# Kernel tuning notes

Hardware: AMD Instinct MI355X
Metric: run time of the kernel (lower is better)

Reference implementation:

```python
import jax, jax.numpy as jnp
import numpy as np

IN_CH = 128
OUT_CH = 256
KSIZE = 3
DOWN = 2
WSCALE_GAIN = 1.0
LR_MUL = 1.0
ACT_GAIN = float(np.sqrt(2.0))  # lrelu def_gain
CONV_CLAMP = 256.0
LRELU_SLOPE = 0.2


def _setup_filter():
    # upfirdn2d.setup_filter([1,3,3,1]): normalize 1D then outer product -> 2D
    f1 = jnp.asarray([1.0, 3.0, 3.0, 1.0], dtype=jnp.float32)
    f1 = f1 / jnp.sum(f1)
    f2 = jnp.outer(f1, f1)  # [4,4]
    return f2


def setup_inputs() -> dict:
    key = jax.random.key(0)
    k1, k2 = jax.random.split(key)
    x = jax.random.normal(k1, (16, IN_CH, 256, 256), dtype=jnp.float32)
    weight = jax.random.normal(k2, (OUT_CH, IN_CH, KSIZE, KSIZE), dtype=jnp.float32)
    bias = jnp.zeros((OUT_CH,), dtype=jnp.float32)
    return {"x": x, "weight": weight, "bias": bias}


def reference(x, weight, bias):
    # runtime_gain = 1.0
    fan_in = KSIZE * KSIZE * IN_CH
    wscale = WSCALE_GAIN / np.sqrt(fan_in) * LR_MUL  # use_wscale=True
    w = weight * jnp.float32(wscale)
    b = bias * jnp.float32(LR_MUL)

    # filter_padding for k=3, fh=fw=4, down=2 -> (2,2,2,2) as (left,right,top,bottom)
    pad = (KSIZE // 2 + (4 - DOWN + 1) // 2, KSIZE // 2 + (4 - DOWN) // 2)
    # upfirdn2d(x, f, down=1, padding): pad then correlate with flipped filter
    f2 = _setup_filter()
    f2 = f2[::-1, ::-1]  # flip (symmetric here, kept for faithfulness)
    C = x.shape[1]
    fk = jnp.broadcast_to(f2[None, None], (C, 1, 4, 4))  # depthwise kernel
    x = lax.pad_fn(x, pad) if False else jnp.pad(x, ((0, 0), (0, 0), (pad[1], pad[0]) if False else (pad[0], pad[1]), (pad[0], pad[1])))
    x = jax.lax.conv_general_dilated(
        x, fk, window_strides=(1, 1), padding='VALID',
        dimension_numbers=('NCHW', 'OIHW', 'NCHW'),
        feature_group_count=C)

    # strided conv2d, padding=0, stride=down
    x = jax.lax.conv_general_dilated(
        x, w, window_strides=(DOWN, DOWN), padding='VALID',
        dimension_numbers=('NCHW', 'OIHW', 'NCHW'))

    # fused bias + lrelu + gain + clamp
    x = x + b[None, :, None, None]
    x = jnp.where(x >= 0, x, x * jnp.float32(LRELU_SLOPE)) * jnp.float32(ACT_GAIN)
    x = jnp.clip(x, -jnp.float32(CONV_CLAMP), jnp.float32(CONV_CLAMP))
    return x
```

## Files before the change

kernel.cpp:

```cpp
#include <hip/hip_runtime.h>

typedef __attribute__((ext_vector_type(8))) short bf16x8;
typedef __attribute__((ext_vector_type(4))) float f32x4;
typedef __attribute__((ext_vector_type(2))) float f32x2;

static __device__ __forceinline__ unsigned short f2bf(float f) {
    union { float f; unsigned u; } v; v.f = f;
    return (unsigned short)((v.u + 0x7FFFu + ((v.u >> 16) & 1u)) >> 16);
}

__global__ void prep_weights(const float* __restrict__ w, unsigned short* __restrict__ wp) {
    int t = blockIdx.x * 256 + threadIdx.x;
    const float wscale = 0.02946278254943948f;
    int cw = t & 31;
    int oc = (t >> 5) & 255;
    int cr = t >> 13;
    int ch = cr / 9;
    int rs = cr - ch * 9;
    int r  = rs / 3;
    int s  = rs - r * 3;
    int c  = ch * 32 + cw;
    wp[t] = f2bf(w[((oc * 128 + c) * 3 + r) * 3 + s] * wscale);
}

#define FROW(row) {                                                            \
    int xr  = xr0 + (row);                                                     \
    int xrc = xr < 0 ? 0 : (xr > 255 ? 255 : xr);                              \
    float rm = (xr == xrc) ? 0.125f : 0.0f;                                    \
    const float* p = q + (xrc << 8);                                           \
    f32x4 lo; f32x2 hi;                                                        \
    __builtin_memcpy(&lo, p, 16);                                              \
    __builtin_memcpy(&hi, p + 4, 8);                                           \
    hA[(row) & 3] = (lo.x + 3.f * (lo.y + lo.z) + lo.w) * rm;                  \
    hB[(row) & 3] = (lo.y + 3.f * (lo.z + lo.w) + hi.x) * rm;                  \
    hC[(row) & 3] = (lo.z + 3.f * (lo.w + hi.x) + hi.y) * rm;                  \
}

#define SROW(row) {                                                            \
    int xr = xr0 + (row);                                                      \
    float wv0=0.f,wv1=0.f,wv2=0.f,wv3=0.f,wv4=0.f,wv5=0.f;                     \
    if ((unsigned)xr < 256u) {                                                 \
        const float* p = q + (xr << 8);                                        \
        if ((unsigned)(wc + 0) < 256u) wv0 = p[0];                             \
        if ((unsigned)(wc + 1) < 256u) wv1 = p[1];                             \
        if ((unsigned)(wc + 2) < 256u) wv2 = p[2];                             \
        if ((unsigned)(wc + 3) < 256u) wv3 = p[3];                             \
        if ((unsigned)(wc + 4) < 256u) wv4 = p[4];                             \
        if ((unsigned)(wc + 5) < 256u) wv5 = p[5];                             \
    }                                                                          \
    hA[(row) & 3] = (wv0 + 3.f * (wv1 + wv2) + wv3) * 0.125f;                  \
    hB[(row) & 3] = (wv1 + 3.f * (wv2 + wv3) + wv4) * 0.125f;                  \
    hC[(row) & 3] = (wv2 + 3.f * (wv3 + wv4) + wv5) * 0.125f;                  \
}

#define VROW(row) {                                                            \
    float bv0 = (hA[(row - 3) & 3] + 3.f * (hA[(row - 2) & 3] + hA[(row - 1) & 3]) + hA[(row) & 3]) * 0.125f; \
    float bv1 = (hB[(row - 3) & 3] + 3.f * (hB[(row - 2) & 3] + hB[(row - 1) & 3]) + hB[(row) & 3]) * 0.125f; \
    unsigned rb = (unsigned)(row - 3) * 2640u;                                 \
    *(unsigned short*)(lds + rb + o0) = f2bf(bv0);                             \
    *(unsigned short*)(lds + rb + o1) = f2bf(bv1);                             \
    if (a == 15) {                                                             \
        float bv2 = (hC[(row - 3) & 3] + 3.f * (hC[(row - 2) & 3] + hC[(row - 1) & 3]) + hC[(row) & 3]) * 0.125f; \
        *(unsigned short*)(lds + rb + o2) = f2bf(bv2);                         \
    }                                                                          \
}

__global__ __launch_bounds__(512, 4)
void conv_blur_mfma(const float* __restrict__ x, const unsigned short* __restrict__ wp,
                    const float* __restrict__ bias, float* __restrict__ out) {
    __shared__ __align__(16) unsigned char lds[17 * 33 * 80];

    const int bx = blockIdx.x;
    const int n  = bx >> 7;
    const int tt = bx & 127;
    const int u0 = (tt >> 3) * 8;
    const int v0 = (tt & 7) * 16;

    const int tid  = threadIdx.x;
    const int lane = tid & 63;
    const int wid  = tid >> 6;
    const int wm   = wid >> 2;
    const int wn   = wid & 3;
    const int g    = lane >> 4;
    const int wq   = lane & 15;

    const int a   = tid & 15;
    const int chl = tid >> 4;
    const int c0  = 2 * a;
    const int wc  = 2 * v0 - 2 + c0;
    const bool edge = (v0 == 0 && a == 0) || (v0 == 112 && a == 15);
    const float* planeBase = x + (size_t)(n * 128 + chl) * 65536;
    const int xr0 = 2 * u0 - 2;

    const unsigned chpart = (unsigned)(((chl >> 1) & 3) * 4 + (chl & 1) * 2);
    const unsigned q4 = (unsigned)(chl >> 3);
    const unsigned o0 = (unsigned)(c0 + 0) * 80u + ((q4 ^ (((unsigned)(c0 + 0) >> 3) & 3u)) << 4) + chpart;
    const unsigned o1 = (unsigned)(c0 + 1) * 80u + ((q4 ^ (((unsigned)(c0 + 1) >> 3) & 3u)) << 4) + chpart;
    const unsigned o2 = (unsigned)(c0 + 2) * 80u + ((q4 ^ (((unsigned)(c0 + 2) >> 3) & 3u)) << 4) + chpart;

    const unsigned short* wpL = wp + (size_t)(wn * 64 + wq) * 32 + g * 8;

    f32x4 acc[4][4];
    #pragma unroll
    for (int i = 0; i < 4; ++i)
        #pragma unroll
        for (int j = 0; j < 4; ++j)
            acc[i][j] = (f32x4){0.f, 0.f, 0.f, 0.f};

    for (int ch = 0; ch < 4; ++ch) {
        const float* q = planeBase + (size_t)ch * 32 * 65536 + wc;
        float hA[4], hB[4], hC[4];
        if (!edge) { FROW(0) FROW(1) FROW(2) }
        else       { SROW(0) SROW(1) SROW(2) }
        __syncthreads();
        if (!edge) {
            #pragma unroll
            for (int row = 3; row < 20; ++row) { FROW(row) VROW(row) }
        } else {
            #pragma unroll
            for (int row = 3; row < 20; ++row) { SROW(row) VROW(row) }
        }
        __syncthreads();
        const unsigned short* wpc = wpL + (size_t)ch * 9 * 8192;
        #pragma unroll 1
        for (int r = 0; r < 3; ++r) {
            #pragma unroll 1
            for (int s = 0; s < 3; ++s) {
                bf16x8 b0 = *(const bf16x8*)(wpc + 0 * 512);
                bf16x8 b1 = *(const bf16x8*)(wpc + 1 * 512);
                bf16x8 b2 = *(const bf16x8*)(wpc + 2 * 512);
                bf16x8 b3 = *(const bf16x8*)(wpc + 3 * 512);
                wpc += 8192;
                int bj = 2 * wq + s;
                unsigned cb = (unsigned)bj * 80u
                            + ((unsigned)(g ^ ((bj >> 3) & 3)) << 4);
                #pragma unroll
                for (int mf = 0; mf < 4; ++mf) {
                    int bi = 2 * (wm * 4 + mf) + r;
                    bf16x8 afrag = *(const bf16x8*)(lds + (unsigned)bi * 2640u + cb);
                    acc[mf][0] = __builtin_amdgcn_mfma_f32_16x16x32_bf16(afrag, b0, acc[mf][0], 0, 0, 0);
                    acc[mf][1] = __builtin_amdgcn_mfma_f32_16x16x32_bf16(afrag, b1, acc[mf][1], 0, 0, 0);
                    acc[mf][2] = __builtin_amdgcn_mfma_f32_16x16x32_bf16(afrag, b2, acc[mf][2], 0, 0, 0);
                    acc[mf][3] = __builtin_amdgcn_mfma_f32_16x16x32_bf16(afrag, b3, acc[mf][3], 0, 0, 0);
                }
            }
        }
    }

    const float gain = 1.4142135623730951f;
    #pragma unroll
    for (int nf = 0; nf < 4; ++nf) {
        int ocg = wn * 64 + nf * 16 + wq;
        float bv = bias[ocg];
        #pragma unroll
        for (int mf = 0; mf < 4; ++mf) {
            int u = u0 + wm * 4 + mf;
            f32x4 o;
            #pragma unroll
            for (int i = 0; i < 4; ++i) {
                float z = acc[mf][nf][i] + bv;
                z = (z >= 0.f ? z : 0.2f * z) * gain;
                o[i] = fminf(fmaxf(z, -256.f), 256.f);
            }
            *(f32x4*)(out + (((size_t)n * 256 + ocg) * 128 + u) * 128 + v0 + 4 * g) = o;
        }
    }
}

extern "C" void kernel_launch(void* const* d_in, const int* in_sizes, int n_in,
                              void* d_out, int out_size, void* d_ws, size_t ws_size,
                              hipStream_t stream) {
    const float* x    = (const float*)d_in[0];
    const float* w    = (const float*)d_in[1];
    const float* bias = (const float*)d_in[2];
    unsigned short* wp = (unsigned short*)d_ws;
    float* out = (float*)d_out;

    prep_weights<<<1152, 256, 0, stream>>>(w, wp);
    conv_blur_mfma<<<2048, 512, 0, stream>>>(x, wp, bias, out);
}
```

Before: 483.5 us.

## Split blur into separate pre-pass writing bf16 channel-interleaved tensor, pipeline conv stage

Adds a blur_pre kernel that computes the 4x4 FIR blur once per input pixel and stores it as bf16 in a swizzled channel-interleaved global buffer in workspace. A new conv_stage2 kernel stages tiles of that buffer into LDS with register prefetch of the next channel group, and double-buffers weight fragments across unrolled MFMA steps with setprio. The fused kernel is kept as a fallback when the workspace is too small. This removes the blur arithmetic repeated by every conv block and hides load latency. The cost is an extra ~270MB round trip through HBM.

```diff
diff --git a/kernel.cpp b/kernel.cpp
--- a/kernel.cpp
+++ b/kernel.cpp
@@ -3,6 +3,7 @@
 typedef __attribute__((ext_vector_type(8))) short bf16x8;
 typedef __attribute__((ext_vector_type(4))) float f32x4;
 typedef __attribute__((ext_vector_type(2))) float f32x2;
+typedef __attribute__((ext_vector_type(4))) unsigned int u32x4;
 
 static __device__ __forceinline__ unsigned short f2bf(float f) {
     union { float f; unsigned u; } v; v.f = f;
@@ -23,6 +24,261 @@
     wp[t] = f2bf(w[((oc * 128 + c) * 3 + r) * 3 + s] * wscale);
 }
 
+
+__global__ void blur_pre(const float* __restrict__ x, unsigned char* __restrict__ bl) {
+    const int b   = blockIdx.x;
+    const int tid = threadIdx.x;
+    const int c   = tid & 31;
+    if (b < 64) {
+        const int n = b >> 2, cg = b & 3;
+        const float* xp = x + (size_t)(n * 128 + cg * 32 + c) * 65536;
+        unsigned char* ob = bl + (size_t)(n * 4 + cg) * 4260096;
+        const int eb = tid >> 5;
+        const float fw0 = 1.f, fw1 = 3.f, fw2 = 3.f, fw3 = 1.f;
+        for (int e = eb; e < 513; e += 8) {
+            int t, J;
+            if (e < 257) { t = e; J = 256; } else { t = 256; J = e - 257; }
+            float acc = 0.f;
+            #pragma unroll
+            for (int p = 0; p < 4; ++p) {
+                int xr = t - 2 + p;
+                if ((unsigned)xr < 256u) {
+                    const float* rp = xp + (xr << 8);
+                    float fp = (p == 0) ? fw0 : (p == 1) ? fw1 : (p == 2) ? fw2 : fw3;
+                    #pragma unroll
+                    for (int q = 0; q < 4; ++q) {
+                        int xc = J - 2 + q;
+                        float fq = (q == 0) ? fw0 : (q == 1) ? fw1 : (q == 2) ? fw2 : fw3;
+                        if ((unsigned)xc < 256u) acc += fp * fq * rp[xc];
+                    }
+                }
+            }
+            acc *= 0.015625f;
+            unsigned off = (unsigned)(J ^ ((J >> 1) & 1)) * 64u
+                         + ((unsigned)((c >> 3) ^ ((J >> 2) & 3)) << 4) + (unsigned)(c & 7) * 2u;
+            *(unsigned short*)(ob + (size_t)t * 16512 + off) = f2bf(acc);
+        }
+        return;
+    }
+    const int b2 = b - 64;
+    const int tband = b2 & 15, band = (b2 >> 4) & 3, cg = (b2 >> 6) & 3, n = b2 >> 8;
+    const int cb = tid >> 5;
+    const int J0 = band * 64 + cb * 8;
+    const int t0 = tband * 16;
+    const bool edge = (J0 == 0) || (J0 == 248);
+    const float* xp = x + (size_t)(n * 128 + cg * 32 + c) * 65536;
+    unsigned char* ob = bl + (size_t)(n * 4 + cg) * 4260096;
+    unsigned off[8];
+    #pragma unroll
+    for (int j = 0; j < 8; ++j) {
+        int J = J0 + j;
+        off[j] = (unsigned)(J ^ ((J >> 1) & 1)) * 64u
+               + ((unsigned)((c >> 3) ^ ((J >> 2) & 3)) << 4) + (unsigned)(c & 7) * 2u;
+    }
+    float h[8][4];
+    #pragma unroll
+    for (int i = 0; i < 19; ++i) {
+        int xr = t0 - 2 + i;
+        if (!edge) {
+            int xc = xr < 0 ? 0 : (xr > 255 ? 255 : xr);
+            float rm = (xr == xc) ? 0.125f : 0.f;
+            const float* p = xp + (xc << 8) + (J0 - 2);
+            f32x4 w0, w1, w2;
+            __builtin_memcpy(&w0, p, 16);
+            __builtin_memcpy(&w1, p + 4, 16);
+            __builtin_memcpy(&w2, p + 8, 16);
+            float wv[12] = {w0.x, w0.y, w0.z, w0.w, w1.x, w1.y, w1.z, w1.w,
+                            w2.x, w2.y, w2.z, w2.w};
+            #pragma unroll
+            for (int j = 0; j < 8; ++j)
+                h[j][i & 3] = (wv[j] + 3.f * (wv[j + 1] + wv[j + 2]) + wv[j + 3]) * rm;
+        } else {
+            float wv[12];
+            #pragma unroll
+            for (int m = 0; m < 12; ++m) {
+                int xc2 = J0 - 2 + m;
+                wv[m] = ((unsigned)xr < 256u && (unsigned)xc2 < 256u)
+                        ? xp[(xr << 8) + xc2] : 0.f;
+            }
+            #pragma unroll
+            for (int j = 0; j < 8; ++j)
+                h[j][i & 3] = (wv[j] + 3.f * (wv[j + 1] + wv[j + 2]) + wv[j + 3]) * 0.125f;
+        }
+        if (i >= 3) {
+            unsigned char* rowp = ob + (size_t)(t0 + i - 3) * 16512;
+            #pragma unroll
+            for (int j = 0; j < 8; ++j) {
+                float B = (h[j][(i - 3) & 3] + 3.f * (h[j][(i - 2) & 3] + h[j][(i - 1) & 3])
+                           + h[j][i & 3]) * 0.125f;
+                *(unsigned short*)(rowp + off[j]) = f2bf(B);
+            }
+        }
+    }
+}
+
+#define MF __builtin_amdgcn_mfma_f32_16x16x32_bf16
+#define WLOAD(S0, S1, S2, S3, KOFF) {                                          \
+    const unsigned short* _wn = wbase + (size_t)(KOFF) * 8192;                 \
+    S0 = *(const bf16x8*)(_wn);        S1 = *(const bf16x8*)(_wn + 512);       \
+    S2 = *(const bf16x8*)(_wn + 1024); S3 = *(const bf16x8*)(_wn + 1536);      \
+}
+#define CSTEP(ADRS, R, S0, S1, S2, S3) {                                       \
+    const unsigned char* _ab = lds + (ADRS) + (R) * 2112;                      \
+    bf16x8 a0 = *(const bf16x8*)(_ab);                                         \
+    bf16x8 a1 = *(const bf16x8*)(_ab + 4224);                                  \
+    bf16x8 a2 = *(const bf16x8*)(_ab + 8448);                                  \
+    bf16x8 a3 = *(const bf16x8*)(_ab + 12672);                                 \
+    __builtin_amdgcn_s_setprio(1);                                             \
+    acc[0][0]=MF(a0,S0,acc[0][0],0,0,0); acc[0][1]=MF(a0,S1,acc[0][1],0,0,0);  \
+    acc[0][2]=MF(a0,S2,acc[0][2],0,0,0); acc[0][3]=MF(a0,S3,acc[0][3],0,0,0);  \
+    acc[1][0]=MF(a1,S0,acc[1][0],0,0,0); acc[1][1]=MF(a1,S1,acc[1][1],0,0,0);  \
+    acc[1][2]=MF(a1,S2,acc[1][2],0,0,0); acc[1][3]=MF(a1,S3,acc[1][3],0,0,0);  \
+    acc[2][0]=MF(a2,S0,acc[2][0],0,0,0); acc[2][1]=MF(a2,S1,acc[2][1],0,0,0);  \
+    acc[2][2]=MF(a2,S2,acc[2][2],0,0,0); acc[2][3]=MF(a2,S3,acc[2][3],0,0,0);  \
+    acc[3][0]=MF(a3,S0,acc[3][0],0,0,0); acc[3][1]=MF(a3,S1,acc[3][1],0,0,0);  \
+    acc[3][2]=MF(a3,S2,acc[3][2],0,0,0); acc[3][3]=MF(a3,S3,acc[3][3],0,0,0);  \
+    __builtin_amdgcn_s_setprio(0);                                             \
+}
+#define CHUNK(BASE, A0,A1,A2,A3, B0,B1,B2,B3)                                  \
+    CSTEP(adr0, 0, A0,A1,A2,A3) WLOAD(A0,A1,A2,A3, (BASE)+2)                   \
+    CSTEP(adr1, 0, B0,B1,B2,B3) WLOAD(B0,B1,B2,B3, (BASE)+3)                   \
+    CSTEP(adr2, 0, A0,A1,A2,A3) WLOAD(A0,A1,A2,A3, (BASE)+4)                   \
+    CSTEP(adr0, 1, B0,B1,B2,B3) WLOAD(B0,B1,B2,B3, (BASE)+5)                   \
+    CSTEP(adr1, 1, A0,A1,A2,A3) WLOAD(A0,A1,A2,A3, (BASE)+6)                   \
+    CSTEP(adr2, 1, B0,B1,B2,B3) WLOAD(B0,B1,B2,B3, (BASE)+7)                   \
+    CSTEP(adr0, 2, A0,A1,A2,A3) WLOAD(A0,A1,A2,A3, (BASE)+8)                   \
+    CSTEP(adr1, 2, B0,B1,B2,B3) WLOAD(B0,B1,B2,B3, (BASE)+9)                   \
+    CSTEP(adr2, 2, A0,A1,A2,A3) WLOAD(A0,A1,A2,A3, (BASE)+10)
+#define CHUNK_LAST(BASE, A0,A1,A2,A3, B0,B1,B2,B3)                             \
+    CSTEP(adr0, 0, A0,A1,A2,A3) WLOAD(A0,A1,A2,A3, (BASE)+2)                   \
+    CSTEP(adr1, 0, B0,B1,B2,B3) WLOAD(B0,B1,B2,B3, (BASE)+3)                   \
+    CSTEP(adr2, 0, A0,A1,A2,A3) WLOAD(A0,A1,A2,A3, (BASE)+4)                   \
+    CSTEP(adr0, 1, B0,B1,B2,B3) WLOAD(B0,B1,B2,B3, (BASE)+5)                   \
+    CSTEP(adr1, 1, A0,A1,A2,A3) WLOAD(A0,A1,A2,A3, (BASE)+6)                   \
+    CSTEP(adr2, 1, B0,B1,B2,B3) WLOAD(B0,B1,B2,B3, (BASE)+7)                   \
+    CSTEP(adr0, 2, A0,A1,A2,A3) WLOAD(A0,A1,A2,A3, (BASE)+8)                   \
+    CSTEP(adr1, 2, B0,B1,B2,B3)                                                \
+    CSTEP(adr2, 2, A0,A1,A2,A3)
+
+__global__ __launch_bounds__(512, 3)
+void conv_stage2(const unsigned char* __restrict__ bl, const unsigned short* __restrict__ wp,
+                 const float* __restrict__ bias, float* __restrict__ out) {
+    __shared__ __align__(16) unsigned char lds[35904];
+
+    const int bx = blockIdx.x;
+    const int n  = bx >> 7;
+    const int tt = bx & 127;
+    const int u0 = (tt >> 3) * 8;
+    const int v0 = (tt & 7) * 16;
+
+    const int tid  = threadIdx.x;
+    const int lane = tid & 63;
+    const int wid  = tid >> 6;
+    const int wm   = wid >> 2;
+    const int wn   = wid & 3;
+    const int g    = lane >> 4;
+    const int wq   = lane & 15;
+
+    unsigned goff[5];
+    #pragma unroll
+    for (int k = 0; k < 5; ++k) {
+        int sl  = tid + 512 * k;
+        int row = sl / 132;
+        int cs  = sl - row * 132;
+        goff[k] = (unsigned)(2 * u0 + row) * 16512u + (unsigned)v0 * 128u + (unsigned)cs * 16u;
+    }
+    const bool v4 = (tid < 196);
+    const unsigned char* gb = bl + (size_t)n * 4 * 4260096;
+
+    unsigned adr0, adr1, adr2;
+    {
+        #pragma unroll
+        for (int s = 0; s < 3; ++s) {
+            unsigned bj = 2u * (unsigned)wq + (unsigned)s;
+            unsigned av = (bj ^ ((bj >> 1) & 1u)) * 64u
+                        + (((unsigned)g ^ ((bj >> 2) & 3u)) << 4) + (unsigned)wm * 16896u;
+            if (s == 0) adr0 = av; else if (s == 1) adr1 = av; else adr2 = av;
+        }
+    }
+
+    const unsigned short* wbase = wp + (size_t)(wn * 64 + wq) * 32 + g * 8;
+    bf16x8 WA0, WA1, WA2, WA3, WB0, WB1, WB2, WB3;
+    WLOAD(WA0, WA1, WA2, WA3, 0)
+    WLOAD(WB0, WB1, WB2, WB3, 1)
+
+    f32x4 acc[4][4];
+    #pragma unroll
+    for (int i = 0; i < 4; ++i)
+        #pragma unroll
+        for (int j = 0; j < 4; ++j)
+            acc[i][j] = (f32x4){0.f, 0.f, 0.f, 0.f};
+
+    u32x4 L0, L1, L2, L3, L4 = (u32x4){0u, 0u, 0u, 0u};
+    {
+        const unsigned char* g0 = gb;
+        L0 = *(const u32x4*)(g0 + goff[0]);
+        L1 = *(const u32x4*)(g0 + goff[1]);
+        L2 = *(const u32x4*)(g0 + goff[2]);
+        L3 = *(const u32x4*)(g0 + goff[3]);
+        if (v4) L4 = *(const u32x4*)(g0 + goff[4]);
+    }
+    const unsigned lb = (unsigned)tid * 16u;
+
+#define STAGE_WRITE() {                                                        \
+    *(u32x4*)(lds + lb)          = L0;                                         \
+    *(u32x4*)(lds + lb + 8192)   = L1;                                         \
+    *(u32x4*)(lds + lb + 16384)  = L2;                                         \
+    *(u32x4*)(lds + lb + 24576)  = L3;                                         \
+    if (v4) *(u32x4*)(lds + lb + 32768) = L4;                                  \
+}
+#define STAGE_LOAD(CGN) {                                                      \
+    const unsigned char* _gn = gb + (size_t)(CGN) * 4260096;                   \
+    L0 = *(const u32x4*)(_gn + goff[0]);                                       \
+    L1 = *(const u32x4*)(_gn + goff[1]);                                       \
+    L2 = *(const u32x4*)(_gn + goff[2]);                                       \
+    L3 = *(const u32x4*)(_gn + goff[3]);                                       \
+    if (v4) L4 = *(const u32x4*)(_gn + goff[4]);                               \
+}
+
+    STAGE_WRITE()
+    __syncthreads();
+    STAGE_LOAD(1)
+    CHUNK(0, WA0, WA1, WA2, WA3, WB0, WB1, WB2, WB3)
+    __syncthreads();
+    STAGE_WRITE()
+    __syncthreads();
+    STAGE_LOAD(2)
+    CHUNK(9, WB0, WB1, WB2, WB3, WA0, WA1, WA2, WA3)
+    __syncthreads();
+    STAGE_WRITE()
+    __syncthreads();
+    STAGE_LOAD(3)
+    CHUNK(18, WA0, WA1, WA2, WA3, WB0, WB1, WB2, WB3)
+    __syncthreads();
+    STAGE_WRITE()
+    __syncthreads();
+    CHUNK_LAST(27, WB0, WB1, WB2, WB3, WA0, WA1, WA2, WA3)
+
+    const float gain = 1.4142135623730951f;
+    #pragma unroll
+    for (int nf = 0; nf < 4; ++nf) {
+        const int ocg = wn * 64 + nf * 16 + wq;
+        const float bb = bias[ocg];
+        #pragma unroll
+        for (int mf = 0; mf < 4; ++mf) {
+            int u = u0 + wm * 4 + mf;
+            f32x4 o;
+            #pragma unroll
+            for (int i = 0; i < 4; ++i) {
+                float z = acc[mf][nf][i] + bb;
+                z = (z >= 0.f ? z : 0.2f * z) * gain;
+                o[i] = fminf(fmaxf(z, -256.f), 256.f);
+            }
+            *(f32x4*)(out + (((size_t)n * 256 + ocg) * 128 + u) * 128 + v0 + 4 * g) = o;
+        }
+    }
+}
+
 #define FROW(row) {                                                            \
     int xr  = xr0 + (row);                                                     \
     int xrc = xr < 0 ? 0 : (xr > 255 ? 255 : xr);                              \
@@ -35,7 +291,6 @@
     hB[(row) & 3] = (lo.y + 3.f * (lo.z + lo.w) + hi.x) * rm;                  \
     hC[(row) & 3] = (lo.z + 3.f * (lo.w + hi.x) + hi.y) * rm;                  \
 }
-
 #define SROW(row) {                                                            \
     int xr = xr0 + (row);                                                      \
     float wv0=0.f,wv1=0.f,wv2=0.f,wv3=0.f,wv4=0.f,wv5=0.f;                     \
@@ -52,30 +307,26 @@
     hB[(row) & 3] = (wv1 + 3.f * (wv2 + wv3) + wv4) * 0.125f;                  \
     hC[(row) & 3] = (wv2 + 3.f * (wv3 + wv4) + wv5) * 0.125f;                  \
 }
-
 #define VROW(row) {                                                            \
     float bv0 = (hA[(row - 3) & 3] + 3.f * (hA[(row - 2) & 3] + hA[(row - 1) & 3]) + hA[(row) & 3]) * 0.125f; \
     float bv1 = (hB[(row - 3) & 3] + 3.f * (hB[(row - 2) & 3] + hB[(row - 1) & 3]) + hB[(row) & 3]) * 0.125f; \
     unsigned rb = (unsigned)(row - 3) * 2640u;                                 \
-    *(unsigned short*)(lds + rb + o0) = f2bf(bv0);                             \
-    *(unsigned short*)(lds + rb + o1) = f2bf(bv1);                             \
+    *(unsigned short*)(flds + rb + o0) = f2bf(bv0);                            \
+    *(unsigned short*)(flds + rb + o1) = f2bf(bv1);                            \
     if (a == 15) {                                                             \
         float bv2 = (hC[(row - 3) & 3] + 3.f * (hC[(row - 2) & 3] + hC[(row - 1) & 3]) + hC[(row) & 3]) * 0.125f; \
-        *(unsigned short*)(lds + rb + o2) = f2bf(bv2);                         \
+        *(unsigned short*)(flds + rb + o2) = f2bf(bv2);                        \
     }                                                                          \
 }
-
 __global__ __launch_bounds__(512, 4)
 void conv_blur_mfma(const float* __restrict__ x, const unsigned short* __restrict__ wp,
                     const float* __restrict__ bias, float* __restrict__ out) {
-    __shared__ __align__(16) unsigned char lds[17 * 33 * 80];
-
+    __shared__ __align__(16) unsigned char flds[17 * 33 * 80];
     const int bx = blockIdx.x;
     const int n  = bx >> 7;
     const int tt = bx & 127;
     const int u0 = (tt >> 3) * 8;
     const int v0 = (tt & 7) * 16;
-
     const int tid  = threadIdx.x;
     const int lane = tid & 63;
     const int wid  = tid >> 6;
@@ -83,30 +334,25 @@
     const int wn   = wid & 3;
     const int g    = lane >> 4;
     const int wq   = lane & 15;
-
     const int a   = tid & 15;
     const int chl = tid >> 4;
-    const int c0  = 2 * a;
-    const int wc  = 2 * v0 - 2 + c0;
+    const int wc  = 2 * v0 - 2 + 2 * a;
     const bool edge = (v0 == 0 && a == 0) || (v0 == 112 && a == 15);
     const float* planeBase = x + (size_t)(n * 128 + chl) * 65536;
     const int xr0 = 2 * u0 - 2;
-
     const unsigned chpart = (unsigned)(((chl >> 1) & 3) * 4 + (chl & 1) * 2);
     const unsigned q4 = (unsigned)(chl >> 3);
+    const int c0 = 2 * a;
     const unsigned o0 = (unsigned)(c0 + 0) * 80u + ((q4 ^ (((unsigned)(c0 + 0) >> 3) & 3u)) << 4) + chpart;
     const unsigned o1 = (unsigned)(c0 + 1) * 80u + ((q4 ^ (((unsigned)(c0 + 1) >> 3) & 3u)) << 4) + chpart;
     const unsigned o2 = (unsigned)(c0 + 2) * 80u + ((q4 ^ (((unsigned)(c0 + 2) >> 3) & 3u)) << 4) + chpart;
-
     const unsigned short* wpL = wp + (size_t)(wn * 64 + wq) * 32 + g * 8;
-
     f32x4 acc[4][4];
     #pragma unroll
     for (int i = 0; i < 4; ++i)
         #pragma unroll
         for (int j = 0; j < 4; ++j)
             acc[i][j] = (f32x4){0.f, 0.f, 0.f, 0.f};
-
     for (int ch = 0; ch < 4; ++ch) {
         const float* q = planeBase + (size_t)ch * 32 * 65536 + wc;
         float hA[4], hB[4], hC[4];
@@ -132,21 +378,19 @@
                 bf16x8 b3 = *(const bf16x8*)(wpc + 3 * 512);
                 wpc += 8192;
                 int bj = 2 * wq + s;
-                unsigned cb = (unsigned)bj * 80u
-                            + ((unsigned)(g ^ ((bj >> 3) & 3)) << 4);
+                unsigned cb = (unsigned)bj * 80u + ((unsigned)(g ^ ((bj >> 3) & 3)) << 4);
                 #pragma unroll
                 for (int mf = 0; mf < 4; ++mf) {
                     int bi = 2 * (wm * 4 + mf) + r;
-                    bf16x8 afrag = *(const bf16x8*)(lds + (unsigned)bi * 2640u + cb);
-                    acc[mf][0] = __builtin_amdgcn_mfma_f32_16x16x32_bf16(afrag, b0, acc[mf][0], 0, 0, 0);
-                    acc[mf][1] = __builtin_amdgcn_mfma_f32_16x16x32_bf16(afrag, b1, acc[mf][1], 0, 0, 0);
-                    acc[mf][2] = __builtin_amdgcn_mfma_f32_16x16x32_bf16(afrag, b2, acc[mf][2], 0, 0, 0);
-                    acc[mf][3] = __builtin_amdgcn_mfma_f32_16x16x32_bf16(afrag, b3, acc[mf][3], 0, 0, 0);
+                    bf16x8 afrag = *(const bf16x8*)(flds + (unsigned)bi * 2640u + cb);
+                    acc[mf][0] = MF(afrag, b0, acc[mf][0], 0, 0, 0);
+                    acc[mf][1] = MF(afrag, b1, acc[mf][1], 0, 0, 0);
+                    acc[mf][2] = MF(afrag, b2, acc[mf][2], 0, 0, 0);
+                    acc[mf][3] = MF(afrag, b3, acc[mf][3], 0, 0, 0);
                 }
             }
         }
     }
-
     const float gain = 1.4142135623730951f;
     #pragma unroll
     for (int nf = 0; nf < 4; ++nf) {
@@ -176,6 +420,13 @@
     unsigned short* wp = (unsigned short*)d_ws;
     float* out = (float*)d_out;
 
+    const size_t NEED = 589824u + 272646144u;
     prep_weights<<<1152, 256, 0, stream>>>(w, wp);
-    conv_blur_mfma<<<2048, 512, 0, stream>>>(x, wp, bias, out);
-}
+    if (ws_size >= NEED) {
+        unsigned char* bl = (unsigned char*)d_ws + 589824;
+        blur_pre<<<4160, 256, 0, stream>>>(x, bl);
+        conv_stage2<<<2048, 512, 0, stream>>>(bl, wp, bias, out);
+    } else {
+        conv_blur_mfma<<<2048, 512, 0, stream>>>(x, wp, bias, out);
+    }
+}
```

Result: slower. 563.2 us (+16.5%).

## Split blur into separate pass and double-buffer conv tiles via direct global-to-LDS loads

Applied to the files above, without the earlier changes.

The fused blur+conv kernel is split in two. A blur pass writes pre-swizzled bf16 tile records to workspace, and a conv kernel streams those records into double-buffered LDS with global_load_lds while running MFMAs on the previous chunk. The conv kernel also changes warp tiling to 8x2 fragments per wave, prefetches weights in registers, and raises wave priority around the MFMA bursts. This costs an extra round trip of about 294 MB through global memory, and the new path only runs if the workspace is large enough.

```diff
diff --git a/kernel.cpp b/kernel.cpp
--- a/kernel.cpp
+++ b/kernel.cpp
@@ -3,10 +3,17 @@
 typedef __attribute__((ext_vector_type(8))) short bf16x8;
 typedef __attribute__((ext_vector_type(4))) float f32x4;
 typedef __attribute__((ext_vector_type(2))) float f32x2;
+typedef __attribute__((ext_vector_type(4))) unsigned int u32x4;
 
 static __device__ __forceinline__ unsigned short f2bf(float f) {
     union { float f; unsigned u; } v; v.f = f;
     return (unsigned short)((v.u + 0x7FFFu + ((v.u >> 16) & 1u)) >> 16);
+}
+
+static __device__ __forceinline__ void g2l16(const void* g, void* l) {
+    __builtin_amdgcn_global_load_lds(
+        (const __attribute__((address_space(1))) unsigned int*)g,
+        (__attribute__((address_space(3))) unsigned int*)l, 16, 0, 0);
 }
 
 __global__ void prep_weights(const float* __restrict__ w, unsigned short* __restrict__ wp) {
@@ -23,6 +30,244 @@
     wp[t] = f2bf(w[((oc * 128 + c) * 3 + r) * 3 + s] * wscale);
 }
 
+#define BPX(ROW) {                                                             \
+    int _xr = xr0 + (ROW);                                                     \
+    int _xc = _xr < 0 ? 0 : (_xr > 255 ? 255 : _xr);                           \
+    float _rm = (_xr == _xc) ? 0.125f : 0.0f;                                  \
+    const float* _p0 = pq0 + (_xc << 8);                                       \
+    const float* _p1 = pq1 + (_xc << 8);                                       \
+    f32x4 _l0, _l1; f32x2 _h0, _h1;                                            \
+    __builtin_memcpy(&_l0, _p0, 16); __builtin_memcpy(&_h0, _p0 + 4, 8);       \
+    __builtin_memcpy(&_l1, _p1, 16); __builtin_memcpy(&_h1, _p1 + 4, 8);       \
+    hA0[(ROW) & 3] = (_l0.x + 3.f * (_l0.y + _l0.z) + _l0.w) * _rm;            \
+    hB0[(ROW) & 3] = (_l0.y + 3.f * (_l0.z + _l0.w) + _h0.x) * _rm;            \
+    hC0[(ROW) & 3] = (_l0.z + 3.f * (_l0.w + _h0.x) + _h0.y) * _rm;            \
+    hA1[(ROW) & 3] = (_l1.x + 3.f * (_l1.y + _l1.z) + _l1.w) * _rm;            \
+    hB1[(ROW) & 3] = (_l1.y + 3.f * (_l1.z + _l1.w) + _h1.x) * _rm;            \
+    hC1[(ROW) & 3] = (_l1.z + 3.f * (_l1.w + _h1.x) + _h1.y) * _rm;            \
+}
+#define BPS(ROW) {                                                             \
+    int _xr = xr0 + (ROW);                                                     \
+    float a0=0.f,a1=0.f,a2=0.f,a3=0.f,a4=0.f,a5=0.f;                           \
+    float b0=0.f,b1=0.f,b2=0.f,b3=0.f,b4=0.f,b5=0.f;                           \
+    if ((unsigned)_xr < 256u) {                                                \
+        const float* _p0 = pq0 + (_xr << 8);                                   \
+        const float* _p1 = pq1 + (_xr << 8);                                   \
+        if ((unsigned)(wc + 0) < 256u) { a0 = _p0[0]; b0 = _p1[0]; }           \
+        if ((unsigned)(wc + 1) < 256u) { a1 = _p0[1]; b1 = _p1[1]; }           \
+        if ((unsigned)(wc + 2) < 256u) { a2 = _p0[2]; b2 = _p1[2]; }           \
+        if ((unsigned)(wc + 3) < 256u) { a3 = _p0[3]; b3 = _p1[3]; }           \
+        if ((unsigned)(wc + 4) < 256u) { a4 = _p0[4]; b4 = _p1[4]; }           \
+        if ((unsigned)(wc + 5) < 256u) { a5 = _p0[5]; b5 = _p1[5]; }           \
+    }                                                                          \
+    hA0[(ROW) & 3] = (a0 + 3.f * (a1 + a2) + a3) * 0.125f;                     \
+    hB0[(ROW) & 3] = (a1 + 3.f * (a2 + a3) + a4) * 0.125f;                     \
+    hC0[(ROW) & 3] = (a2 + 3.f * (a3 + a4) + a5) * 0.125f;                     \
+    hA1[(ROW) & 3] = (b0 + 3.f * (b1 + b2) + b3) * 0.125f;                     \
+    hB1[(ROW) & 3] = (b1 + 3.f * (b2 + b3) + b4) * 0.125f;                     \
+    hC1[(ROW) & 3] = (b2 + 3.f * (b3 + b4) + b5) * 0.125f;                     \
+}
+#define BPV(ROW) {                                                             \
+    float vA0 = (hA0[(ROW-3)&3] + 3.f*(hA0[(ROW-2)&3]+hA0[(ROW-1)&3]) + hA0[(ROW)&3]) * 0.125f; \
+    float vA1 = (hA1[(ROW-3)&3] + 3.f*(hA1[(ROW-2)&3]+hA1[(ROW-1)&3]) + hA1[(ROW)&3]) * 0.125f; \
+    float vB0 = (hB0[(ROW-3)&3] + 3.f*(hB0[(ROW-2)&3]+hB0[(ROW-1)&3]) + hB0[(ROW)&3]) * 0.125f; \
+    float vB1 = (hB1[(ROW-3)&3] + 3.f*(hB1[(ROW-2)&3]+hB1[(ROW-1)&3]) + hB1[(ROW)&3]) * 0.125f; \
+    unsigned _rb = (unsigned)(ROW - 3) * 2112u;                                \
+    *(unsigned*)(blds + _rb + o0) = (unsigned)f2bf(vA0) | ((unsigned)f2bf(vA1) << 16); \
+    *(unsigned*)(blds + _rb + o1) = (unsigned)f2bf(vB0) | ((unsigned)f2bf(vB1) << 16); \
+    if (a15) {                                                                 \
+        float vC0 = (hC0[(ROW-3)&3] + 3.f*(hC0[(ROW-2)&3]+hC0[(ROW-1)&3]) + hC0[(ROW)&3]) * 0.125f; \
+        float vC1 = (hC1[(ROW-3)&3] + 3.f*(hC1[(ROW-2)&3]+hC1[(ROW-1)&3]) + hC1[(ROW)&3]) * 0.125f; \
+        *(unsigned*)(blds + _rb + o2) = (unsigned)f2bf(vC0) | ((unsigned)f2bf(vC1) << 16); \
+    }                                                                          \
+}
+#define BPF(ROW) BPX(ROW) BPV(ROW)
+#define BPP(ROW) BPS(ROW) BPV(ROW)
+
+__global__ __launch_bounds__(256, 4)
+void blur_rec(const float* __restrict__ x, unsigned char* __restrict__ bm) {
+    __shared__ __align__(16) unsigned char blds[35904];
+    const int bx   = blockIdx.x;
+    const int cg   = bx & 3;
+    const int tile = (bx >> 2) & 127;
+    const int n    = bx >> 9;
+    const int u0   = (tile >> 3) * 8;
+    const int v0   = (tile & 7) * 16;
+    const int tid  = threadIdx.x;
+    const int a    = tid & 15;
+    const int chp  = tid >> 4;
+    const bool a15 = (a == 15);
+    const int wc   = 2 * v0 - 2 + 2 * a;
+    const bool edge = (v0 == 0 && a == 0) || (v0 == 112 && a15);
+    const float* pq0 = x + (size_t)(n * 128 + cg * 32 + 2 * chp) * 65536 + wc;
+    const float* pq1 = pq0 + 65536;
+    const int xr0 = 2 * u0 - 2;
+
+    const int J0 = 2 * a, J1 = 2 * a + 1;
+    const unsigned cb2 = (unsigned)(chp & 3) * 4u;
+    const unsigned o0 = (unsigned)((J0 ^ ((J0 >> 1) & 1)) * 64) + ((((unsigned)chp >> 2) ^ (((unsigned)J0 >> 2) & 3u)) << 4) + cb2;
+    const unsigned o1 = (unsigned)((J1 ^ ((J1 >> 1) & 1)) * 64) + ((((unsigned)chp >> 2) ^ (((unsigned)J1 >> 2) & 3u)) << 4) + cb2;
+    const unsigned o2 = 2048u + (((unsigned)chp >> 2) << 4) + cb2;
+
+    {
+        float hA0[4], hB0[4], hC0[4], hA1[4], hB1[4], hC1[4];
+        if (!edge) {
+            BPX(0) BPX(1) BPX(2)
+            BPF(3)  BPF(4)  BPF(5)  BPF(6)  BPF(7)  BPF(8)  BPF(9)  BPF(10)
+            BPF(11) BPF(12) BPF(13) BPF(14) BPF(15) BPF(16) BPF(17) BPF(18) BPF(19)
+        } else {
+            BPS(0) BPS(1) BPS(2)
+            BPP(3)  BPP(4)  BPP(5)  BPP(6)  BPP(7)  BPP(8)  BPP(9)  BPP(10)
+            BPP(11) BPP(12) BPP(13) BPP(14) BPP(15) BPP(16) BPP(17) BPP(18) BPP(19)
+        }
+    }
+    __syncthreads();
+    unsigned char* dst = bm + (size_t)bx * 35904u;
+    #pragma unroll
+    for (int k = 0; k < 8; ++k)
+        *(u32x4*)(dst + (unsigned)(tid + 256 * k) * 16u) =
+            *(const u32x4*)(blds + (unsigned)(tid + 256 * k) * 16u);
+    if (tid < 196)
+        *(u32x4*)(dst + (unsigned)(tid + 2048) * 16u) =
+            *(const u32x4*)(blds + (unsigned)(tid + 2048) * 16u);
+}
+
+#define MF __builtin_amdgcn_mfma_f32_16x16x32_bf16
+#define WLOAD2(S0, S1, KOFF) {                                                 \
+    const unsigned short* _wn = wbase + (size_t)(KOFF) * 8192;                 \
+    S0 = *(const bf16x8*)(_wn); S1 = *(const bf16x8*)(_wn + 512);              \
+}
+#define CSTEP8(BUF, ADRS, R, S0, S1) {                                         \
+    const unsigned char* _ab = lds + (BUF) + (ADRS) + (R) * 2112;              \
+    bf16x8 a0 = *(const bf16x8*)(_ab);                                         \
+    bf16x8 a1 = *(const bf16x8*)(_ab +  4224);                                 \
+    bf16x8 a2 = *(const bf16x8*)(_ab +  8448);                                 \
+    bf16x8 a3 = *(const bf16x8*)(_ab + 12672);                                 \
+    bf16x8 a4 = *(const bf16x8*)(_ab + 16896);                                 \
+    bf16x8 a5 = *(const bf16x8*)(_ab + 21120);                                 \
+    bf16x8 a6 = *(const bf16x8*)(_ab + 25344);                                 \
+    bf16x8 a7 = *(const bf16x8*)(_ab + 29568);                                 \
+    __builtin_amdgcn_s_setprio(1);                                             \
+    acc[0][0]=MF(a0,S0,acc[0][0],0,0,0); acc[0][1]=MF(a0,S1,acc[0][1],0,0,0);  \
+    acc[1][0]=MF(a1,S0,acc[1][0],0,0,0); acc[1][1]=MF(a1,S1,acc[1][1],0,0,0);  \
+    acc[2][0]=MF(a2,S0,acc[2][0],0,0,0); acc[2][1]=MF(a2,S1,acc[2][1],0,0,0);  \
+    acc[3][0]=MF(a3,S0,acc[3][0],0,0,0); acc[3][1]=MF(a3,S1,acc[3][1],0,0,0);  \
+    acc[4][0]=MF(a4,S0,acc[4][0],0,0,0); acc[4][1]=MF(a4,S1,acc[4][1],0,0,0);  \
+    acc[5][0]=MF(a5,S0,acc[5][0],0,0,0); acc[5][1]=MF(a5,S1,acc[5][1],0,0,0);  \
+    acc[6][0]=MF(a6,S0,acc[6][0],0,0,0); acc[6][1]=MF(a6,S1,acc[6][1],0,0,0);  \
+    acc[7][0]=MF(a7,S0,acc[7][0],0,0,0); acc[7][1]=MF(a7,S1,acc[7][1],0,0,0);  \
+    __builtin_amdgcn_s_setprio(0);                                             \
+}
+#define CHUNK8(BUF, BASE, A0,A1, B0,B1)                                        \
+    CSTEP8(BUF, adr0, 0, A0,A1) WLOAD2(A0,A1, (BASE)+2)                        \
+    CSTEP8(BUF, adr1, 0, B0,B1) WLOAD2(B0,B1, (BASE)+3)                        \
+    CSTEP8(BUF, adr2, 0, A0,A1) WLOAD2(A0,A1, (BASE)+4)                        \
+    CSTEP8(BUF, adr0, 1, B0,B1) WLOAD2(B0,B1, (BASE)+5)                        \
+    CSTEP8(BUF, adr1, 1, A0,A1) WLOAD2(A0,A1, (BASE)+6)                        \
+    CSTEP8(BUF, adr2, 1, B0,B1) WLOAD2(B0,B1, (BASE)+7)                        \
+    CSTEP8(BUF, adr0, 2, A0,A1) WLOAD2(A0,A1, (BASE)+8)                        \
+    CSTEP8(BUF, adr1, 2, B0,B1) WLOAD2(B0,B1, (BASE)+9)                        \
+    CSTEP8(BUF, adr2, 2, A0,A1) WLOAD2(A0,A1, (BASE)+10)
+#define CHUNK8_LAST(BUF, BASE, A0,A1, B0,B1)                                   \
+    CSTEP8(BUF, adr0, 0, A0,A1) WLOAD2(A0,A1, (BASE)+2)                        \
+    CSTEP8(BUF, adr1, 0, B0,B1) WLOAD2(B0,B1, (BASE)+3)                        \
+    CSTEP8(BUF, adr2, 0, A0,A1) WLOAD2(A0,A1, (BASE)+4)                        \
+    CSTEP8(BUF, adr0, 1, B0,B1) WLOAD2(B0,B1, (BASE)+5)                        \
+    CSTEP8(BUF, adr1, 1, A0,A1) WLOAD2(A0,A1, (BASE)+6)                        \
+    CSTEP8(BUF, adr2, 1, B0,B1) WLOAD2(B0,B1, (BASE)+7)                        \
+    CSTEP8(BUF, adr0, 2, A0,A1) WLOAD2(A0,A1, (BASE)+8)                        \
+    CSTEP8(BUF, adr1, 2, B0,B1)                                                \
+    CSTEP8(BUF, adr2, 2, A0,A1)
+
+__global__ __launch_bounds__(512, 4)
+void conv_stage2(const unsigned char* __restrict__ bm, const unsigned short* __restrict__ wp,
+                 const float* __restrict__ bias, float* __restrict__ out) {
+    __shared__ __align__(16) unsigned char lds[2 * 35904];
+
+    const int bx = blockIdx.x;
+    const int n  = bx >> 7;
+    const int tt = bx & 127;
+    const int u0 = (tt >> 3) * 8;
+    const int v0 = (tt & 7) * 16;
+
+    const int tid  = threadIdx.x;
+    const int lane = tid & 63;
+    const int wid  = tid >> 6;
+    const int g    = lane >> 4;
+    const int wq   = lane & 15;
+
+    const unsigned char* rec = bm + (size_t)((n * 128 + tt) * 4) * 35904u;
+
+#define STAGE(BUF, CG) {                                                       \
+    const unsigned char* _src = rec + (size_t)(CG) * 35904u;                   \
+    _Pragma("unroll")                                                          \
+    for (int k = 0; k < 4; ++k)                                                \
+        g2l16(_src + (unsigned)(tid + 512 * k) * 16u,                          \
+              lds + (BUF) + (unsigned)(tid + 512 * k) * 16u);                  \
+    if (tid < 196)                                                             \
+        g2l16(_src + (unsigned)(tid + 2048) * 16u,                             \
+              lds + (BUF) + (unsigned)(tid + 2048) * 16u);                     \
+}
+
+    unsigned adr0, adr1, adr2;
+    {
+        #pragma unroll
+        for (int s = 0; s < 3; ++s) {
+            unsigned bj = 2u * (unsigned)wq + (unsigned)s;
+            unsigned av = (bj ^ ((bj >> 1) & 1u)) * 64u
+                        + (((unsigned)g ^ ((bj >> 2) & 3u)) << 4);
+            if (s == 0) adr0 = av; else if (s == 1) adr1 = av; else adr2 = av;
+        }
+    }
+
+    const unsigned short* wbase = wp + (size_t)(wid * 32 + wq) * 32 + g * 8;
+    bf16x8 WA0, WA1, WB0, WB1;
+    WLOAD2(WA0, WA1, 0)
+    WLOAD2(WB0, WB1, 1)
+
+    f32x4 acc[8][2];
+    #pragma unroll
+    for (int i = 0; i < 8; ++i) {
+        acc[i][0] = (f32x4){0.f, 0.f, 0.f, 0.f};
+        acc[i][1] = (f32x4){0.f, 0.f, 0.f, 0.f};
+    }
+
+    STAGE(0, 0)
+    __syncthreads();
+
+    STAGE(35904, 1)
+    CHUNK8(0, 0, WA0, WA1, WB0, WB1)
+    __syncthreads();
+
+    STAGE(0, 2)
+    CHUNK8(35904, 9, WB0, WB1, WA0, WA1)
+    __syncthreads();
+
+    STAGE(35904, 3)
+    CHUNK8(0, 18, WA0, WA1, WB0, WB1)
+    __syncthreads();
+
+    CHUNK8_LAST(35904, 27, WB0, WB1, WA0, WA1)
+
+    const float gain = 1.4142135623730951f;
+    #pragma unroll
+    for (int nf = 0; nf < 2; ++nf) {
+        const int ocg = wid * 32 + nf * 16 + wq;
+        const float bb = bias[ocg];
+        #pragma unroll
+        for (int mf = 0; mf < 8; ++mf) {
+            f32x4 o;
+            #pragma unroll
+            for (int i = 0; i < 4; ++i) {
+                float z = acc[mf][nf][i] + bb;
+                z = (z >= 0.f ? z : 0.2f * z) * gain;
+                o[i] = fminf(fmaxf(z, -256.f), 256.f);
+            }
+            *(f32x4*)(out + (((size_t)n * 256 + ocg) * 128 + (u0 + mf)) * 128 + v0 + 4 * g) = o;
+        }
+    }
+}
+
 #define FROW(row) {                                                            \
     int xr  = xr0 + (row);                                                     \
     int xrc = xr < 0 ? 0 : (xr > 255 ? 255 : xr);                              \
@@ -35,7 +280,6 @@
     hB[(row) & 3] = (lo.y + 3.f * (lo.z + lo.w) + hi.x) * rm;                  \
     hC[(row) & 3] = (lo.z + 3.f * (lo.w + hi.x) + hi.y) * rm;                  \
 }
-
 #define SROW(row) {                                                            \
     int xr = xr0 + (row);                                                      \
     float wv0=0.f,wv1=0.f,wv2=0.f,wv3=0.f,wv4=0.f,wv5=0.f;                     \
@@ -52,30 +296,26 @@
     hB[(row) & 3] = (wv1 + 3.f * (wv2 + wv3) + wv4) * 0.125f;                  \
     hC[(row) & 3] = (wv2 + 3.f * (wv3 + wv4) + wv5) * 0.125f;                  \
 }
-
 #define VROW(row) {                                                            \
     float bv0 = (hA[(row - 3) & 3] + 3.f * (hA[(row - 2) & 3] + hA[(row - 1) & 3]) + hA[(row) & 3]) * 0.125f; \
     float bv1 = (hB[(row - 3) & 3] + 3.f * (hB[(row - 2) & 3] + hB[(row - 1) & 3]) + hB[(row) & 3]) * 0.125f; \
     unsigned rb = (unsigned)(row - 3) * 2640u;                                 \
-    *(unsigned short*)(lds + rb + o0) = f2bf(bv0);                             \
-    *(unsigned short*)(lds + rb + o1) = f2bf(bv1);                             \
+    *(unsigned short*)(flds + rb + o0) = f2bf(bv0);                            \
+    *(unsigned short*)(flds + rb + o1) = f2bf(bv1);                            \
     if (a == 15) {                                                             \
         float bv2 = (hC[(row - 3) & 3] + 3.f * (hC[(row - 2) & 3] + hC[(row - 1) & 3]) + hC[(row) & 3]) * 0.125f; \
-        *(unsigned short*)(lds + rb + o2) = f2bf(bv2);                         \
+        *(unsigned short*)(flds + rb + o2) = f2bf(bv2);                        \
     }                                                                          \
 }
-
 __global__ __launch_bounds__(512, 4)
 void conv_blur_mfma(const float* __restrict__ x, const unsigned short* __restrict__ wp,
                     const float* __restrict__ bias, float* __restrict__ out) {
-    __shared__ __align__(16) unsigned char lds[17 * 33 * 80];
-
+    __shared__ __align__(16) unsigned char flds[17 * 33 * 80];
     const int bx = blockIdx.x;
     const int n  = bx >> 7;
     const int tt = bx & 127;
     const int u0 = (tt >> 3) * 8;
     const int v0 = (tt & 7) * 16;
-
     const int tid  = threadIdx.x;
     const int lane = tid & 63;
     const int wid  = tid >> 6;
@@ -83,30 +323,25 @@
     const int wn   = wid & 3;
     const int g    = lane >> 4;
     const int wq   = lane & 15;
-
     const int a   = tid & 15;
     const int chl = tid >> 4;
-    const int c0  = 2 * a;
-    const int wc  = 2 * v0 - 2 + c0;
+    const int wc  = 2 * v0 - 2 + 2 * a;
     const bool edge = (v0 == 0 && a == 0) || (v0 == 112 && a == 15);
     const float* planeBase = x + (size_t)(n * 128 + chl) * 65536;
     const int xr0 = 2 * u0 - 2;
-
     const unsigned chpart = (unsigned)(((chl >> 1) & 3) * 4 + (chl & 1) * 2);
     const unsigned q4 = (unsigned)(chl >> 3);
+    const int c0 = 2 * a;
     const unsigned o0 = (unsigned)(c0 + 0) * 80u + ((q4 ^ (((unsigned)(c0 + 0) >> 3) & 3u)) << 4) + chpart;
     const unsigned o1 = (unsigned)(c0 + 1) * 80u + ((q4 ^ (((unsigned)(c0 + 1) >> 3) & 3u)) << 4) + chpart;
     const unsigned o2 = (unsigned)(c0 + 2) * 80u + ((q4 ^ (((unsigned)(c0 + 2) >> 3) & 3u)) << 4) + chpart;
-
     const unsigned short* wpL = wp + (size_t)(wn * 64 + wq) * 32 + g * 8;
-
     f32x4 acc[4][4];
     #pragma unroll
     for (int i = 0; i < 4; ++i)
         #pragma unroll
         for (int j = 0; j < 4; ++j)
             acc[i][j] = (f32x4){0.f, 0.f, 0.f, 0.f};
-
     for (int ch = 0; ch < 4; ++ch) {
         const float* q = planeBase + (size_t)ch * 32 * 65536 + wc;
         float hA[4], hB[4], hC[4];
@@ -132,21 +367,19 @@
                 bf16x8 b3 = *(const bf16x8*)(wpc + 3 * 512);
                 wpc += 8192;
                 int bj = 2 * wq + s;
-                unsigned cb = (unsigned)bj * 80u
-                            + ((unsigned)(g ^ ((bj >> 3) & 3)) << 4);
+                unsigned cb = (unsigned)bj * 80u + ((unsigned)(g ^ ((bj >> 3) & 3)) << 4);
                 #pragma unroll
                 for (int mf = 0; mf < 4; ++mf) {
                     int bi = 2 * (wm * 4 + mf) + r;
-                    bf16x8 afrag = *(const bf16x8*)(lds + (unsigned)bi * 2640u + cb);
-                    acc[mf][0] = __builtin_amdgcn_mfma_f32_16x16x32_bf16(afrag, b0, acc[mf][0], 0, 0, 0);
-                    acc[mf][1] = __builtin_amdgcn_mfma_f32_16x16x32_bf16(afrag, b1, acc[mf][1], 0, 0, 0);
-                    acc[mf][2] = __builtin_amdgcn_mfma_f32_16x16x32_bf16(afrag, b2, acc[mf][2], 0, 0, 0);
-                    acc[mf][3] = __builtin_amdgcn_mfma_f32_16x16x32_bf16(afrag, b3, acc[mf][3], 0, 0, 0);
+                    bf16x8 afrag = *(const bf16x8*)(flds + (unsigned)bi * 2640u + cb);
+                    acc[mf][0] = MF(afrag, b0, acc[mf][0], 0, 0, 0);
+                    acc[mf][1] = MF(afrag, b1, acc[mf][1], 0, 0, 0);
+                    acc[mf][2] = MF(afrag, b2, acc[mf][2], 0, 0, 0);
+                    acc[mf][3] = MF(afrag, b3, acc[mf][3], 0, 0, 0);
                 }
             }
         }
     }
-
     const float gain = 1.4142135623730951f;
     #pragma unroll
     for (int nf = 0; nf < 4; ++nf) {
@@ -176,6 +409,14 @@
     unsigned short* wp = (unsigned short*)d_ws;
     float* out = (float*)d_out;
 
+    const size_t BM_BYTES = (size_t)8192 * 35904u;
+    const size_t NEED = 589824u + BM_BYTES;
     prep_weights<<<1152, 256, 0, stream>>>(w, wp);
-    conv_blur_mfma<<<2048, 512, 0, stream>>>(x, wp, bias, out);
-}
+    if (ws_size >= NEED) {
+        unsigned char* bm = (unsigned char*)d_ws + 589824;
+        blur_rec<<<8192, 256, 0, stream>>>(x, bm);
+        conv_stage2<<<2048, 512, 0, stream>>>(bm, wp, bias, out);
+    } else {
+        conv_blur_mfma<<<2048, 512, 0, stream>>>(x, wp, bias, out);
+    }
+}
```

New measurement: 476.7 us. About the same (-1.4%).
